# Optimization experiments

Measured on AMD Instinct MI355X. Metric: run time of the kernel, lower is better.

Reference implementation:

```python
import jax, jax.numpy as jnp
import numpy as np

EPS_BN = 1e-5


def _batchnorm(h, g, b):
    # training-mode BatchNorm1d over the flattened (B*N*k) axis
    mu = jnp.mean(h, axis=0)
    var = jnp.var(h, axis=0)
    return g * (h - mu) * jax.lax.rsqrt(var + EPS_BN) + b


def setup_inputs() -> dict:
    key = jax.random.key(0)
    ks = jax.random.split(key, 5)
    B, N = 4, 8192
    x = jax.random.normal(ks[0], (B, N, 3), dtype=jnp.float32)
    W1 = jax.random.normal(ks[1], (7, 10), dtype=jnp.float32) * (1.0 / np.sqrt(7.0))
    b1 = jax.random.normal(ks[2], (10,), dtype=jnp.float32) * 0.01
    W2 = jax.random.normal(ks[3], (10, 10), dtype=jnp.float32) * (1.0 / np.sqrt(10.0))
    b2 = jax.random.normal(ks[4], (10,), dtype=jnp.float32) * 0.01
    g1 = jnp.ones((10,), jnp.float32); be1 = jnp.zeros((10,), jnp.float32)
    g2 = jnp.ones((10,), jnp.float32); be2 = jnp.zeros((10,), jnp.float32)
    return {"x": x, "W1": W1, "b1": b1, "g1": g1, "be1": be1,
            "W2": W2, "b2": b2, "g2": g2, "be2": be2, "k": 9}


def reference(x, W1, b1, g1, be1, W2, b2, g2, be2, k):
    B, N, C = x.shape
    # --- kNN graph (brute force, self included as nearest) ---
    sq = jnp.sum(x * x, axis=-1)                                    # (B,N)
    d2 = sq[:, :, None] + sq[:, None, :] - 2.0 * jnp.einsum('bnc,bmc->bnm', x, x)
    _, idx = jax.lax.top_k(-d2, k + 1)                              # (B,N,k+1)
    nbrs = x[jnp.arange(B)[:, None, None], idx]                     # (B,N,k+1,3)
    rel = (nbrs - x[:, :, None, :])[:, :, 1:, :]                    # drop self -> (B,N,k,3)
    # --- sort neighbors by azimuth phi = atan2(y, x) ---
    phi = jnp.arctan2(rel[..., 1], rel[..., 0])                     # (B,N,k)
    order = jnp.argsort(phi, axis=-1)
    v1 = jnp.take_along_axis(rel, order[..., None], axis=2)         # (B,N,k,3)
    v2 = jnp.roll(v1, -1, axis=2)                                   # next neighbor (cyclic)
    # --- umbrella-style surface features ---
    centroids = 0.5 * (v1 + v2)
    normals = jnp.cross(v1, v2)
    normals = normals / (jnp.linalg.norm(normals, axis=-1, keepdims=True) + 1e-6)
    sign = jnp.where(normals[..., 0:1, 0] > 0, 1.0, -1.0)[..., None]  # (B,N,1,1)
    normals = normals * sign
    position = jnp.sum(normals * centroids, axis=-1, keepdims=True) / jnp.sqrt(jnp.asarray(3.0, x.dtype))
    feat = jnp.concatenate([centroids, normals, position], axis=-1)   # (B,N,k,7)
    feat = feat.reshape(B * N * k, 7)
    # --- tiny MLP + max-pool over k ---
    h = jax.nn.relu(_batchnorm(feat @ W1 + b1, g1, be1))
    h = jax.nn.relu(_batchnorm(h @ W2 + b2, g2, be2))
    return jnp.max(h.reshape(B, N, k, 10), axis=2)                  # (B,N,10)
```

## Files before the change

### kernel.cpp

```cpp
#include <hip/hip_runtime.h>
#include <math.h>
#include <float.h>
#include <stdint.h>

#define B_ 4
#define N_ 8192
#define K_ 9
#define NPTS (B_ * N_)
#define NROWS (NPTS * K_)
#define SPLIT 8
#define CHUNK (N_ / SPLIT)
#define NGROUP 32
#define GSIZE (CHUNK / NGROUP)
#define GSTRIDE 33
#define NCOPY 16

typedef float f4 __attribute__((ext_vector_type(4)));
typedef float f32x2 __attribute__((ext_vector_type(2)));

__device__ __forceinline__ f32x2 dist2_pk(f32x2 xx, f32x2 yy, f32x2 zz, f32x2 ww,
                                          f32x2 qx, f32x2 qy, f32x2 qz, f32x2 qw) {
  f32x2 t0 = qx * xx;
  f32x2 t1 = __builtin_elementwise_fma(qy, yy, t0);
  f32x2 t2 = __builtin_elementwise_fma(qz, zz, t1);
  f32x2 s  = qw + ww;
  f32x2 m2 = {-2.0f, -2.0f};
  return __builtin_elementwise_fma(t2, m2, s);
}

#define GDECL(G) float gd##G; int gi##G;
#define TOURN8()                                                           \
  float e01d, e23d, e45d, e67d, f03d, f47d, md;                            \
  int   e01i, e23i, e45i, e67i, f03i, f47i, mi;                            \
  { bool t;                                                                \
    t = d1 < d0; e01d = t ? d1 : d0; e01i = t ? (j + 1) : (j + 0);         \
    t = d3 < d2; e23d = t ? d3 : d2; e23i = t ? (j + 3) : (j + 2);         \
    t = d5 < d4; e45d = t ? d5 : d4; e45i = t ? (j + 5) : (j + 4);         \
    t = d7 < d6; e67d = t ? d7 : d6; e67i = t ? (j + 7) : (j + 6);         \
    t = e23d < e01d; f03d = t ? e23d : e01d; f03i = t ? e23i : e01i;       \
    t = e67d < e45d; f47d = t ? e67d : e45d; f47i = t ? e67i : e45i;       \
    t = f47d < f03d; md = t ? f47d : f03d; mi = t ? f47i : f03i; }
#define SCANG(G)                                                           \
  { float bgd = FLT_MAX; int bgi = 0;                                      \
    _Pragma("clang loop unroll(disable)")                                  \
    for (int pr = 0; pr < 16; pr += 4) {                                   \
      const f4* cp = CH + (G * GSTRIDE + 2 * pr);                          \
      f4 A0 = cp[0], B0 = cp[1], A1 = cp[2], B1 = cp[3];                   \
      f4 A2 = cp[4], B2 = cp[5], A3 = cp[6], B3 = cp[7];                   \
      int j = G * GSIZE + 2 * pr;                                          \
      f32x2 dA = dist2_pk(__builtin_shufflevector(A0, A0, 0, 1),           \
                          __builtin_shufflevector(A0, A0, 2, 3),           \
                          __builtin_shufflevector(B0, B0, 0, 1),           \
                          __builtin_shufflevector(B0, B0, 2, 3),           \
                          qx2, qy2, qz2, qw2);                             \
      f32x2 dB = dist2_pk(__builtin_shufflevector(A1, A1, 0, 1),           \
                          __builtin_shufflevector(A1, A1, 2, 3),           \
                          __builtin_shufflevector(B1, B1, 0, 1),           \
                          __builtin_shufflevector(B1, B1, 2, 3),           \
                          qx2, qy2, qz2, qw2);                             \
      f32x2 dC = dist2_pk(__builtin_shufflevector(A2, A2, 0, 1),           \
                          __builtin_shufflevector(A2, A2, 2, 3),           \
                          __builtin_shufflevector(B2, B2, 0, 1),           \
                          __builtin_shufflevector(B2, B2, 2, 3),           \
                          qx2, qy2, qz2, qw2);                             \
      f32x2 dD = dist2_pk(__builtin_shufflevector(A3, A3, 0, 1),           \
                          __builtin_shufflevector(A3, A3, 2, 3),           \
                          __builtin_shufflevector(B3, B3, 0, 1),           \
                          __builtin_shufflevector(B3, B3, 2, 3),           \
                          qx2, qy2, qz2, qw2);                             \
      float d0 = dA.x, d1 = dA.y, d2 = dB.x, d3 = dB.y;                    \
      float d4 = dC.x, d5 = dC.y, d6 = dD.x, d7 = dD.y;                    \
      if (HS) {                                                            \
        d0 = (j + 0 == nl) ? FLT_MAX : d0;                                 \
        d1 = (j + 1 == nl) ? FLT_MAX : d1;                                 \
        d2 = (j + 2 == nl) ? FLT_MAX : d2;                                 \
        d3 = (j + 3 == nl) ? FLT_MAX : d3;                                 \
        d4 = (j + 4 == nl) ? FLT_MAX : d4;                                 \
        d5 = (j + 5 == nl) ? FLT_MAX : d5;                                 \
        d6 = (j + 6 == nl) ? FLT_MAX : d6;                                 \
        d7 = (j + 7 == nl) ? FLT_MAX : d7;                                 \
      }                                                                    \
      TOURN8();                                                            \
      bool lt = md < bgd; bgd = lt ? md : bgd; bgi = lt ? mi : bgi;        \
    }                                                                      \
    gd##G = bgd; gi##G = bgi; }
#define LMC(G, S)                                                          \
  { bool lt = gd##G < wd##S;                                               \
    wd##S = lt ? gd##G : wd##S; wi##S = lt ? gi##G : wi##S;                \
    wg##S = lt ? G : wg##S; }
#define CMB(S)                                                             \
  { bool lt = wd##S < wda;                                                 \
    wda = lt ? wd##S : wda; wia = lt ? wi##S : wia; wga = lt ? wg##S : wga; }
#define WBK(G)                                                             \
  { bool m = (wg == G); gd##G = m ? nd : gd##G; gi##G = m ? ni : gi##G; }

template <bool HS>
__device__ __forceinline__ void knn_chunk(const f4* CH, f32x2 qx2, f32x2 qy2,
                                          f32x2 qz2, f32x2 qw2,
                                          int nl, int j0, int s, int p,
                                          uint2* __restrict__ PBDI) {
  GDECL(0) GDECL(1) GDECL(2) GDECL(3) GDECL(4) GDECL(5) GDECL(6) GDECL(7)
  GDECL(8) GDECL(9) GDECL(10) GDECL(11) GDECL(12) GDECL(13) GDECL(14) GDECL(15)
  GDECL(16) GDECL(17) GDECL(18) GDECL(19) GDECL(20) GDECL(21) GDECL(22) GDECL(23)
  GDECL(24) GDECL(25) GDECL(26) GDECL(27) GDECL(28) GDECL(29) GDECL(30) GDECL(31)

  SCANG(0) SCANG(1) SCANG(2) SCANG(3) SCANG(4) SCANG(5) SCANG(6) SCANG(7)
  SCANG(8) SCANG(9) SCANG(10) SCANG(11) SCANG(12) SCANG(13) SCANG(14) SCANG(15)
  SCANG(16) SCANG(17) SCANG(18) SCANG(19) SCANG(20) SCANG(21) SCANG(22) SCANG(23)
  SCANG(24) SCANG(25) SCANG(26) SCANG(27) SCANG(28) SCANG(29) SCANG(30) SCANG(31)

#pragma clang loop unroll(disable)
  for (int r = 0; r < K_; ++r) {
    float wda = gd0; int wia = gi0; int wga = 0;
    LMC(1,a) LMC(2,a) LMC(3,a) LMC(4,a) LMC(5,a) LMC(6,a) LMC(7,a)
    float wdb = gd8; int wib = gi8; int wgb = 8;
    LMC(9,b) LMC(10,b) LMC(11,b) LMC(12,b) LMC(13,b) LMC(14,b) LMC(15,b)
    float wdc = gd16; int wic = gi16; int wgc = 16;
    LMC(17,c) LMC(18,c) LMC(19,c) LMC(20,c) LMC(21,c) LMC(22,c) LMC(23,c)
    float wdd = gd24; int wid = gi24; int wgd = 24;
    LMC(25,d) LMC(26,d) LMC(27,d) LMC(28,d) LMC(29,d) LMC(30,d) LMC(31,d)
    CMB(b) CMB(c) CMB(d)
    float wd = wda; int wi = wia; int wg = wga;

    uint2 o; o.x = __float_as_uint(wd); o.y = (unsigned)(j0 + wi);
    PBDI[(size_t)(s * K_ + r) * NPTS + p] = o;

    int ab = wg * GSTRIDE;
    int jb = wg * GSIZE;
    float nd = FLT_MAX; int ni = 0;
#pragma clang loop unroll(disable)
    for (int pr = 0; pr < 16; pr += 4) {
      const f4* cp = CH + (ab + 2 * pr);
      f4 A0 = cp[0], B0 = cp[1], A1 = cp[2], B1 = cp[3];
      f4 A2 = cp[4], B2 = cp[5], A3 = cp[6], B3 = cp[7];
      int j = jb + 2 * pr;
      f32x2 dA = dist2_pk(__builtin_shufflevector(A0, A0, 0, 1),
                          __builtin_shufflevector(A0, A0, 2, 3),
                          __builtin_shufflevector(B0, B0, 0, 1),
                          __builtin_shufflevector(B0, B0, 2, 3),
                          qx2, qy2, qz2, qw2);
      f32x2 dB = dist2_pk(__builtin_shufflevector(A1, A1, 0, 1),
                          __builtin_shufflevector(A1, A1, 2, 3),
                          __builtin_shufflevector(B1, B1, 0, 1),
                          __builtin_shufflevector(B1, B1, 2, 3),
                          qx2, qy2, qz2, qw2);
      f32x2 dC = dist2_pk(__builtin_shufflevector(A2, A2, 0, 1),
                          __builtin_shufflevector(A2, A2, 2, 3),
                          __builtin_shufflevector(B2, B2, 0, 1),
                          __builtin_shufflevector(B2, B2, 2, 3),
                          qx2, qy2, qz2, qw2);
      f32x2 dD = dist2_pk(__builtin_shufflevector(A3, A3, 0, 1),
                          __builtin_shufflevector(A3, A3, 2, 3),
                          __builtin_shufflevector(B3, B3, 0, 1),
                          __builtin_shufflevector(B3, B3, 2, 3),
                          qx2, qy2, qz2, qw2);
      float d0 = dA.x, d1 = dA.y, d2 = dB.x, d3 = dB.y;
      float d4 = dC.x, d5 = dC.y, d6 = dD.x, d7 = dD.y;
      if (HS) {
        d0 = (j + 0 == nl) ? FLT_MAX : d0;
        d1 = (j + 1 == nl) ? FLT_MAX : d1;
        d2 = (j + 2 == nl) ? FLT_MAX : d2;
        d3 = (j + 3 == nl) ? FLT_MAX : d3;
        d4 = (j + 4 == nl) ? FLT_MAX : d4;
        d5 = (j + 5 == nl) ? FLT_MAX : d5;
        d6 = (j + 6 == nl) ? FLT_MAX : d6;
        d7 = (j + 7 == nl) ? FLT_MAX : d7;
      }
      bool k0 = (d0 > wd) | ((d0 == wd) & ((j + 0) > wi));
      bool k1 = (d1 > wd) | ((d1 == wd) & ((j + 1) > wi));
      bool k2 = (d2 > wd) | ((d2 == wd) & ((j + 2) > wi));
      bool k3 = (d3 > wd) | ((d3 == wd) & ((j + 3) > wi));
      bool k4 = (d4 > wd) | ((d4 == wd) & ((j + 4) > wi));
      bool k5 = (d5 > wd) | ((d5 == wd) & ((j + 5) > wi));
      bool k6 = (d6 > wd) | ((d6 == wd) & ((j + 6) > wi));
      bool k7 = (d7 > wd) | ((d7 == wd) & ((j + 7) > wi));
      d0 = k0 ? d0 : FLT_MAX;
      d1 = k1 ? d1 : FLT_MAX;
      d2 = k2 ? d2 : FLT_MAX;
      d3 = k3 ? d3 : FLT_MAX;
      d4 = k4 ? d4 : FLT_MAX;
      d5 = k5 ? d5 : FLT_MAX;
      d6 = k6 ? d6 : FLT_MAX;
      d7 = k7 ? d7 : FLT_MAX;
      TOURN8();
      bool lt = md < nd; nd = lt ? md : nd; ni = lt ? mi : ni;
    }
    WBK(0) WBK(1) WBK(2) WBK(3) WBK(4) WBK(5) WBK(6) WBK(7)
    WBK(8) WBK(9) WBK(10) WBK(11) WBK(12) WBK(13) WBK(14) WBK(15)
    WBK(16) WBK(17) WBK(18) WBK(19) WBK(20) WBK(21) WBK(22) WBK(23)
    WBK(24) WBK(25) WBK(26) WBK(27) WBK(28) WBK(29) WBK(30) WBK(31)
  }
}

__launch_bounds__(128, 4)
__global__ void k_knn(const float* __restrict__ x, uint2* __restrict__ PBDI) {
  __shared__ f4 CH[NGROUP * GSTRIDE];
  int bid = blockIdx.x;
  int pg = bid >> 3;
  int s = bid & (SPLIT - 1);
  int p = pg * 128 + threadIdx.x;
  int b = p >> 13;
  int n = p & (N_ - 1);
  int bO = b * N_;
  int j0 = s * CHUNK;

  const float* xq = x + 3 * (size_t)p;
  float qa = xq[0], qb = xq[1], qc = xq[2];
  float qw = qa * qa + qb * qb + qc * qc;
  f32x2 qx2 = {qa, qa}, qy2 = {qb, qb}, qz2 = {qc, qc}, qw2 = {qw, qw};

  for (int u = threadIdx.x; u < CHUNK / 2; u += 128) {
    const float* xp = x + 3 * (size_t)(bO + j0 + 2 * u);
    float a0 = xp[0], b0 = xp[1], c0 = xp[2];
    float a1 = xp[3], b1 = xp[4], c1 = xp[5];
    int G = u >> 4, rr = u & 15;
    f4 lo = {a0, a1, b0, b1};
    f4 hi = {c0, c1, a0 * a0 + b0 * b0 + c0 * c0, a1 * a1 + b1 * b1 + c1 * c1};
    CH[G * GSTRIDE + 2 * rr] = lo;
    CH[G * GSTRIDE + 2 * rr + 1] = hi;
  }
  __syncthreads();

  int n0 = (pg * 128) & (N_ - 1);
  int nl = n - j0;
  if (s == (n0 >> 10)) knn_chunk<true >(CH, qx2, qy2, qz2, qw2, nl, j0, s, p, PBDI);
  else                 knn_chunk<false>(CH, qx2, qy2, qz2, qw2, nl, j0, s, p, PBDI);
}

#define LVL(bdv, biv)                                                     \
  { bool lt = cd < (bdv); float td = (bdv); int ti = (biv);               \
    (bdv) = lt ? cd : (bdv); (biv) = lt ? ci : (biv);                     \
    cd = lt ? td : cd; ci = lt ? ti : ci; }
#define INS9ALL()                                                         \
  LVL(b0d, b0i) LVL(b1d, b1i) LVL(b2d, b2i) LVL(b3d, b3i) LVL(b4d, b4i)  \
  LVL(b5d, b5i) LVL(b6d, b6i) LVL(b7d, b7i) LVL(b8d, b8i)
#define TOP9_DECL()                                                       \
  float b0d = FLT_MAX, b1d = FLT_MAX, b2d = FLT_MAX, b3d = FLT_MAX,       \
        b4d = FLT_MAX, b5d = FLT_MAX, b6d = FLT_MAX, b7d = FLT_MAX,       \
        b8d = FLT_MAX;                                                    \
  int b0i = 0, b1i = 0, b2i = 0, b3i = 0, b4i = 0, b5i = 0, b6i = 0,      \
      b7i = 0, b8i = 0;

#define MKREL(T)                                                          \
  float rx##T, ry##T, rz##T, ph##T;                                       \
  { const float* mp = x + 3 * (size_t)(bO + b##T##i);                     \
    rx##T = mp[0] - qa; ry##T = mp[1] - qb; rz##T = mp[2] - qc;           \
    ph##T = atan2f(ry##T, rx##T); }

#define CE(A, Bv)                                                         \
  { bool lt = ph##Bv < ph##A; float t0;                                   \
    t0 = ph##A; ph##A = lt ? ph##Bv : t0; ph##Bv = lt ? t0 : ph##Bv;      \
    t0 = rx##A; rx##A = lt ? rx##Bv : t0; rx##Bv = lt ? t0 : rx##Bv;      \
    t0 = ry##A; ry##A = lt ? ry##Bv : t0; ry##Bv = lt ? t0 : ry##Bv;      \
    t0 = rz##A; rz##A = lt ? rz##Bv : t0; rz##Bv = lt ? t0 : rz##Bv; }

#define ST9(arr, v0, v1, v2, v3, v4, v5, v6, v7, v8)                      \
  arr[0 * 64 + pl] = v0; arr[1 * 64 + pl] = v1; arr[2 * 64 + pl] = v2;    \
  arr[3 * 64 + pl] = v3; arr[4 * 64 + pl] = v4; arr[5 * 64 + pl] = v5;    \
  arr[6 * 64 + pl] = v6; arr[7 * 64 + pl] = v7; arr[8 * 64 + pl] = v8;

__launch_bounds__(256, 4)
__global__ void k_tail1(const float* __restrict__ x, const uint2* __restrict__ PBDI,
                        const float* __restrict__ W1, const float* __restrict__ b1,
                        float* __restrict__ H1, double* __restrict__ ACC) {
  __shared__ float  LMD[64 * 37];
  __shared__ int    LMI[64 * 37];
  __shared__ float  LREL[3][9 * 64];
  __shared__ float  LSGN[64];
  __shared__ double sred[4][20];

  int q = threadIdx.x >> 6;
  int pl = threadIdx.x & 63;
  int pbase = blockIdx.x * 64;
  int p = pbase + pl;

  {
    TOP9_DECL();
#pragma clang loop unroll_count(2)
    for (int e = 0; e < 2 * K_; ++e) {
      uint2 v = PBDI[(size_t)(q * 2 * K_ + e) * NPTS + p];
      float cd = __uint_as_float(v.x);
      int ci = (int)v.y;
      INS9ALL();
    }
    int base = pl * 37 + q * 9;
    LMD[base + 0] = b0d; LMD[base + 1] = b1d; LMD[base + 2] = b2d;
    LMD[base + 3] = b3d; LMD[base + 4] = b4d; LMD[base + 5] = b5d;
    LMD[base + 6] = b6d; LMD[base + 7] = b7d; LMD[base + 8] = b8d;
    LMI[base + 0] = b0i; LMI[base + 1] = b1i; LMI[base + 2] = b2i;
    LMI[base + 3] = b3i; LMI[base + 4] = b4i; LMI[base + 5] = b5i;
    LMI[base + 6] = b6i; LMI[base + 7] = b7i; LMI[base + 8] = b8i;
  }
  __syncthreads();

  if (q == 0) {
    int b = p >> 13;
    int bO = b * N_;
    const float* xq = x + 3 * (size_t)p;
    float qa = xq[0], qb = xq[1], qc = xq[2];

    TOP9_DECL();
#pragma clang loop unroll_count(3)
    for (int e = 0; e < 4 * K_; ++e) {
      float cd = LMD[pl * 37 + e];
      int ci = LMI[pl * 37 + e];
      INS9ALL();
    }

    MKREL(0) MKREL(1) MKREL(2) MKREL(3) MKREL(4)
    MKREL(5) MKREL(6) MKREL(7) MKREL(8)

    CE(0,1)
    CE(1,2) CE(0,1)
    CE(2,3) CE(1,2) CE(0,1)
    CE(3,4) CE(2,3) CE(1,2) CE(0,1)
    CE(4,5) CE(3,4) CE(2,3) CE(1,2) CE(0,1)
    CE(5,6) CE(4,5) CE(3,4) CE(2,3) CE(1,2) CE(0,1)
    CE(6,7) CE(5,6) CE(4,5) CE(3,4) CE(2,3) CE(1,2) CE(0,1)
    CE(7,8) CE(6,7) CE(5,6) CE(4,5) CE(3,4) CE(2,3) CE(1,2) CE(0,1)

    float nx0 = ry0 * rz1 - rz0 * ry1;
    float ny0 = rz0 * rx1 - rx0 * rz1;
    float nz0 = rx0 * ry1 - ry0 * rx1;
    float nrm0 = sqrtf(nx0 * nx0 + ny0 * ny0 + nz0 * nz0) + 1e-6f;
    LSGN[pl] = ((nx0 / nrm0) > 0.0f) ? 1.0f : -1.0f;

    ST9(LREL[0], rx0, rx1, rx2, rx3, rx4, rx5, rx6, rx7, rx8)
    ST9(LREL[1], ry0, ry1, ry2, ry3, ry4, ry5, ry6, ry7, ry8)
    ST9(LREL[2], rz0, rz1, rz2, rz3, rz4, rz5, rz6, rz7, rz8)
  }
  __syncthreads();

  double sum[10], ss[10];
#pragma unroll
  for (int c = 0; c < 10; ++c) { sum[c] = 0.0; ss[c] = 0.0; }

#pragma clang loop unroll(disable)
  for (int rl = threadIdx.x; rl < 9 * 64; rl += 256) {
    int t = rl >> 6;
    int pp = rl & 63;
    int t2 = (t + 1 == K_) ? 0 : t + 1;
    float v1x = LREL[0][t * 64 + pp];
    float v1y = LREL[1][t * 64 + pp];
    float v1z = LREL[2][t * 64 + pp];
    float v2x = LREL[0][t2 * 64 + pp];
    float v2y = LREL[1][t2 * 64 + pp];
    float v2z = LREL[2][t2 * 64 + pp];
    float sgn = LSGN[pp];

    float cx = 0.5f * (v1x + v2x);
    float cy = 0.5f * (v1y + v2y);
    float cz = 0.5f * (v1z + v2z);
    float nx = v1y * v2z - v1z * v2y;
    float ny = v1z * v2x - v1x * v2z;
    float nz = v1x * v2y - v1y * v2x;
    float nrm = sqrtf(nx * nx + ny * ny + nz * nz) + 1e-6f;
    nx /= nrm; ny /= nrm; nz /= nrm;
    nx *= sgn; ny *= sgn; nz *= sgn;
    float pos = (nx * cx + ny * cy + nz * cz) / 1.7320508075688772f;

    float fv[7] = {cx, cy, cz, nx, ny, nz, pos};
#pragma unroll
    for (int c = 0; c < 10; ++c) {
      float h = b1[c];
#pragma unroll
      for (int rr = 0; rr < 7; ++rr) h = fmaf(fv[rr], W1[rr * 10 + c], h);
      H1[(size_t)c * NROWS + (size_t)t * NPTS + pbase + pp] = h;
      double hd = (double)h;
      sum[c] += hd; ss[c] += hd * hd;
    }
  }

  int lane = threadIdx.x & 63, wv = threadIdx.x >> 6;
#pragma unroll
  for (int c = 0; c < 10; ++c) {
    double a = sum[c];
#pragma unroll
    for (int off = 32; off > 0; off >>= 1) a += __shfl_down(a, off);
    if (lane == 0) sred[wv][c] = a;
    double qq = ss[c];
#pragma unroll
    for (int off = 32; off > 0; off >>= 1) qq += __shfl_down(qq, off);
    if (lane == 0) sred[wv][10 + c] = qq;
  }
  __syncthreads();
  if (threadIdx.x < 20) {
    atomicAdd(&ACC[(blockIdx.x & (NCOPY - 1)) * 40 + threadIdx.x],
              sred[0][threadIdx.x] + sred[1][threadIdx.x] +
              sred[2][threadIdx.x] + sred[3][threadIdx.x]);
  }
}

__launch_bounds__(64)
__global__ void k_mlp2(const float* __restrict__ H1, double* __restrict__ ACC,
                       const float* __restrict__ g1, const float* __restrict__ be1,
                       const float* __restrict__ W2, const float* __restrict__ b2,
                       const float* __restrict__ g2, float* __restrict__ EXT) {
  __shared__ float MR[20];
  __shared__ double sred[20];
  if (threadIdx.x < 20) {
    int c = threadIdx.x % 10;
    int half = threadIdx.x / 10;
    double s0 = 0.0, s1 = 0.0;
#pragma unroll
    for (int cc = 0; cc < NCOPY; ++cc) {
      s0 += ACC[cc * 40 + c];
      s1 += ACC[cc * 40 + 10 + c];
    }
    double mu = s0 / (double)NROWS;
    double var = s1 / (double)NROWS - mu * mu;
    MR[threadIdx.x] = half ? (float)(1.0 / sqrt(var + 1e-5)) : (float)mu;
  }
  __syncthreads();

  int p = blockIdx.x * 64 + threadIdx.x;
  double sum[10], ss[10];
  float ext[10], sg[10];
#pragma unroll
  for (int c = 0; c < 10; ++c) {
    sum[c] = 0.0; ss[c] = 0.0;
    sg[c] = g2[c];
    ext[c] = (sg[c] >= 0.0f) ? -FLT_MAX : FLT_MAX;
  }

#pragma clang loop unroll(disable)
  for (int t = 0; t < K_; ++t) {
    float v[10];
#pragma unroll
    for (int c = 0; c < 10; ++c) {
      float h = H1[(size_t)c * NROWS + (size_t)t * NPTS + p];
      float z = g1[c] * (h - MR[c]) * MR[10 + c] + be1[c];
      v[c] = z > 0.0f ? z : 0.0f;
    }
#pragma unroll
    for (int c = 0; c < 10; ++c) {
      float h = b2[c];
#pragma unroll
      for (int u = 0; u < 10; ++u) h = fmaf(v[u], W2[u * 10 + c], h);
      sum[c] += (double)h;
      ss[c] += (double)h * (double)h;
      ext[c] = (sg[c] >= 0.0f) ? fmaxf(ext[c], h) : fminf(ext[c], h);
    }
  }

#pragma unroll
  for (int c = 0; c < 10; ++c)
    EXT[(size_t)c * NPTS + p] = ext[c];

#pragma unroll
  for (int c = 0; c < 10; ++c) {
    double a = sum[c];
#pragma unroll
    for (int off = 32; off > 0; off >>= 1) a += __shfl_down(a, off);
    if (threadIdx.x == 0) sred[c] = a;
    double qq = ss[c];
#pragma unroll
    for (int off = 32; off > 0; off >>= 1) qq += __shfl_down(qq, off);
    if (threadIdx.x == 0) sred[10 + c] = qq;
  }
  __syncthreads();
  if (threadIdx.x < 20) {
    atomicAdd(&ACC[(blockIdx.x & (NCOPY - 1)) * 40 + 20 + threadIdx.x],
              sred[threadIdx.x]);
  }
}

__launch_bounds__(64)
__global__ void k_out(const float* __restrict__ EXT, const double* __restrict__ ACC,
                      const float* __restrict__ g2, const float* __restrict__ be2,
                      float* __restrict__ out) {
  __shared__ float MR[20];
  if (threadIdx.x < 20) {
    int c = threadIdx.x % 10;
    int half = threadIdx.x / 10;
    double s0 = 0.0, s1 = 0.0;
#pragma unroll
    for (int cc = 0; cc < NCOPY; ++cc) {
      s0 += ACC[cc * 40 + 20 + c];
      s1 += ACC[cc * 40 + 30 + c];
    }
    double mu = s0 / (double)NROWS;
    double var = s1 / (double)NROWS - mu * mu;
    MR[threadIdx.x] = half ? (float)(1.0 / sqrt(var + 1e-5)) : (float)mu;
  }
  __syncthreads();

  int p = blockIdx.x * 64 + threadIdx.x;
#pragma unroll
  for (int c = 0; c < 10; ++c) {
    float h = EXT[(size_t)c * NPTS + p];
    float z = g2[c] * (h - MR[c]) * MR[10 + c] + be2[c];
    z = z > 0.0f ? z : 0.0f;
    out[(size_t)p * 10 + c] = z;
  }
}

extern "C" void kernel_launch(void* const* d_in, const int* in_sizes, int n_in,
                              void* d_out, int out_size, void* d_ws, size_t ws_size,
                              hipStream_t stream) {
  (void)in_sizes; (void)n_in; (void)out_size; (void)ws_size;
  const float* x  = (const float*)d_in[0];
  const float* W1 = (const float*)d_in[1];
  const float* b1 = (const float*)d_in[2];
  const float* g1 = (const float*)d_in[3];
  const float* be1= (const float*)d_in[4];
  const float* W2 = (const float*)d_in[5];
  const float* b2 = (const float*)d_in[6];
  const float* g2 = (const float*)d_in[7];
  const float* be2= (const float*)d_in[8];
  float* out = (float*)d_out;

  char* base = (char*)d_ws;
  uint2*  PBDI = (uint2*)base;
  float*  H1 = (float*)(base + (size_t)SPLIT * K_ * NPTS * 8);
  double* ACC = (double*)(H1 + (size_t)10 * NROWS);
  float*  EXT = (float*)PBDI;

  hipMemsetAsync(ACC, 0, NCOPY * 40 * sizeof(double), stream);
  k_knn<<<(NPTS / 128) * SPLIT, 128, 0, stream>>>(x, PBDI);
  k_tail1<<<NPTS / 64, 256, 0, stream>>>(x, PBDI, W1, b1, H1, ACC);
  k_mlp2<<<NPTS / 64, 64, 0, stream>>>(H1, ACC, g1, be1, W2, b2, g2, EXT);
  k_out<<<NPTS / 64, 64, 0, stream>>>(EXT, ACC, g2, be2, out);
}
```

Baseline: 231.6 us.

## Defer kNN index tracking to winner recompute, fold ACC memset into kernel, unroll loops

The brute-force kNN scan now keeps only the min distance per 8-candidate batch with fminf, plus the batch position, and no longer carries indices through a tournament. Each time a group wins a selection round, its winning batch is recomputed to find the exact index, taking the lowest index on ties. This is meant to cut ALU and register work in the hot distance-scan loop, at the cost of a small extra recompute per selected neighbour. Separately, the ACC zeroing moves from a hipMemsetAsync into block 0 of k_knn to save a launch, and two tail loops are fully unrolled.

```diff
diff --git a/kernel.cpp b/kernel.cpp
--- a/kernel.cpp
+++ b/kernel.cpp
@@ -29,25 +29,13 @@
 }
 
 #define GDECL(G) float gd##G; int gi##G;
-#define TOURN8()                                                           \
-  float e01d, e23d, e45d, e67d, f03d, f47d, md;                            \
-  int   e01i, e23i, e45i, e67i, f03i, f47i, mi;                            \
-  { bool t;                                                                \
-    t = d1 < d0; e01d = t ? d1 : d0; e01i = t ? (j + 1) : (j + 0);         \
-    t = d3 < d2; e23d = t ? d3 : d2; e23i = t ? (j + 3) : (j + 2);         \
-    t = d5 < d4; e45d = t ? d5 : d4; e45i = t ? (j + 5) : (j + 4);         \
-    t = d7 < d6; e67d = t ? d7 : d6; e67i = t ? (j + 7) : (j + 6);         \
-    t = e23d < e01d; f03d = t ? e23d : e01d; f03i = t ? e23i : e01i;       \
-    t = e67d < e45d; f47d = t ? e67d : e45d; f47i = t ? e67i : e45i;       \
-    t = f47d < f03d; md = t ? f47d : f03d; mi = t ? f47i : f03i; }
 #define SCANG(G)                                                           \
-  { float bgd = FLT_MAX; int bgi = 0;                                      \
+  { float bgd = FLT_MAX; int bq = 0;                                       \
     _Pragma("clang loop unroll(disable)")                                  \
     for (int pr = 0; pr < 16; pr += 4) {                                   \
       const f4* cp = CH + (G * GSTRIDE + 2 * pr);                          \
       f4 A0 = cp[0], B0 = cp[1], A1 = cp[2], B1 = cp[3];                   \
       f4 A2 = cp[4], B2 = cp[5], A3 = cp[6], B3 = cp[7];                   \
-      int j = G * GSIZE + 2 * pr;                                          \
       f32x2 dA = dist2_pk(__builtin_shufflevector(A0, A0, 0, 1),           \
                           __builtin_shufflevector(A0, A0, 2, 3),           \
                           __builtin_shufflevector(B0, B0, 0, 1),           \
@@ -71,6 +59,7 @@
       float d0 = dA.x, d1 = dA.y, d2 = dB.x, d3 = dB.y;                    \
       float d4 = dC.x, d5 = dC.y, d6 = dD.x, d7 = dD.y;                    \
       if (HS) {                                                            \
+        int j = G * GSIZE + 2 * pr;                                        \
         d0 = (j + 0 == nl) ? FLT_MAX : d0;                                 \
         d1 = (j + 1 == nl) ? FLT_MAX : d1;                                 \
         d2 = (j + 2 == nl) ? FLT_MAX : d2;                                 \
@@ -80,10 +69,11 @@
         d6 = (j + 6 == nl) ? FLT_MAX : d6;                                 \
         d7 = (j + 7 == nl) ? FLT_MAX : d7;                                 \
       }                                                                    \
-      TOURN8();                                                            \
-      bool lt = md < bgd; bgd = lt ? md : bgd; bgi = lt ? mi : bgi;        \
+      float m = fminf(fminf(fminf(d0, d1), fminf(d2, d3)),                 \
+                      fminf(fminf(d4, d5), fminf(d6, d7)));                \
+      bool lt = m < bgd; bgd = lt ? m : bgd; bq = lt ? pr : bq;            \
     }                                                                      \
-    gd##G = bgd; gi##G = bgi; }
+    gd##G = bgd; gi##G = -1 - bq; }
 #define LMC(G, S)                                                          \
   { bool lt = gd##G < wd##S;                                               \
     wd##S = lt ? gd##G : wd##S; wi##S = lt ? gi##G : wi##S;                \
@@ -93,6 +83,18 @@
     wda = lt ? wd##S : wda; wia = lt ? wi##S : wia; wga = lt ? wg##S : wga; }
 #define WBK(G)                                                             \
   { bool m = (wg == G); gd##G = m ? nd : gd##G; gi##G = m ? ni : gi##G; }
+
+#define TOURN8()                                                           \
+  float e01d, e23d, e45d, e67d, f03d, f47d, md;                            \
+  int   e01i, e23i, e45i, e67i, f03i, f47i, mi;                            \
+  { bool t;                                                                \
+    t = d1 < d0; e01d = t ? d1 : d0; e01i = t ? (j + 1) : (j + 0);         \
+    t = d3 < d2; e23d = t ? d3 : d2; e23i = t ? (j + 3) : (j + 2);         \
+    t = d5 < d4; e45d = t ? d5 : d4; e45i = t ? (j + 5) : (j + 4);         \
+    t = d7 < d6; e67d = t ? d7 : d6; e67i = t ? (j + 7) : (j + 6);         \
+    t = e23d < e01d; f03d = t ? e23d : e01d; f03i = t ? e23i : e01i;       \
+    t = e67d < e45d; f47d = t ? e67d : e45d; f47i = t ? e67i : e45i;       \
+    t = f47d < f03d; md = t ? f47d : f03d; mi = t ? f47i : f03i; }
 
 template <bool HS>
 __device__ __forceinline__ void knn_chunk(const f4* CH, f32x2 qx2, f32x2 qy2,
@@ -120,13 +122,72 @@
     float wdd = gd24; int wid = gi24; int wgd = 24;
     LMC(25,d) LMC(26,d) LMC(27,d) LMC(28,d) LMC(29,d) LMC(30,d) LMC(31,d)
     CMB(b) CMB(c) CMB(d)
-    float wd = wda; int wi = wia; int wg = wga;
+    float wd = wda; int wist = wia; int wg = wga;
+
+    int ab = wg * GSTRIDE;
+    int jb = wg * GSIZE;
+
+    int wi;
+    {
+      int bq = (wist >= 0) ? 0 : (-1 - wist);
+      const f4* cp = CH + (ab + 2 * bq);
+      f4 A0 = cp[0], B0 = cp[1], A1 = cp[2], B1 = cp[3];
+      f4 A2 = cp[4], B2 = cp[5], A3 = cp[6], B3 = cp[7];
+      int j = jb + 2 * bq;
+      f32x2 dA = dist2_pk(__builtin_shufflevector(A0, A0, 0, 1),
+                          __builtin_shufflevector(A0, A0, 2, 3),
+                          __builtin_shufflevector(B0, B0, 0, 1),
+                          __builtin_shufflevector(B0, B0, 2, 3),
+                          qx2, qy2, qz2, qw2);
+      f32x2 dB = dist2_pk(__builtin_shufflevector(A1, A1, 0, 1),
+                          __builtin_shufflevector(A1, A1, 2, 3),
+                          __builtin_shufflevector(B1, B1, 0, 1),
+                          __builtin_shufflevector(B1, B1, 2, 3),
+                          qx2, qy2, qz2, qw2);
+      f32x2 dC = dist2_pk(__builtin_shufflevector(A2, A2, 0, 1),
+                          __builtin_shufflevector(A2, A2, 2, 3),
+                          __builtin_shufflevector(B2, B2, 0, 1),
+                          __builtin_shufflevector(B2, B2, 2, 3),
+                          qx2, qy2, qz2, qw2);
+      f32x2 dD = dist2_pk(__builtin_shufflevector(A3, A3, 0, 1),
+                          __builtin_shufflevector(A3, A3, 2, 3),
+                          __builtin_shufflevector(B3, B3, 0, 1),
+                          __builtin_shufflevector(B3, B3, 2, 3),
+                          qx2, qy2, qz2, qw2);
+      float d0 = dA.x, d1 = dA.y, d2 = dB.x, d3 = dB.y;
+      float d4 = dC.x, d5 = dC.y, d6 = dD.x, d7 = dD.y;
+      if (HS) {
+        d0 = (j + 0 == nl) ? FLT_MAX : d0;
+        d1 = (j + 1 == nl) ? FLT_MAX : d1;
+        d2 = (j + 2 == nl) ? FLT_MAX : d2;
+        d3 = (j + 3 == nl) ? FLT_MAX : d3;
+        d4 = (j + 4 == nl) ? FLT_MAX : d4;
+        d5 = (j + 5 == nl) ? FLT_MAX : d5;
+        d6 = (j + 6 == nl) ? FLT_MAX : d6;
+        d7 = (j + 7 == nl) ? FLT_MAX : d7;
+      }
+      const int IMX = 0x7fffffff;
+      int a0 = (d0 == wd) ? (j + 0) : IMX;
+      int a1 = (d1 == wd) ? (j + 1) : IMX;
+      int a2 = (d2 == wd) ? (j + 2) : IMX;
+      int a3 = (d3 == wd) ? (j + 3) : IMX;
+      int a4 = (d4 == wd) ? (j + 4) : IMX;
+      int a5 = (d5 == wd) ? (j + 5) : IMX;
+      int a6 = (d6 == wd) ? (j + 6) : IMX;
+      int a7 = (d7 == wd) ? (j + 7) : IMX;
+      int m01 = a0 < a1 ? a0 : a1;
+      int m23 = a2 < a3 ? a2 : a3;
+      int m45 = a4 < a5 ? a4 : a5;
+      int m67 = a6 < a7 ? a6 : a7;
+      int mA = m01 < m23 ? m01 : m23;
+      int mB = m45 < m67 ? m45 : m67;
+      int jm = mA < mB ? mA : mB;
+      wi = (wist >= 0) ? wist : jm;
+    }
 
     uint2 o; o.x = __float_as_uint(wd); o.y = (unsigned)(j0 + wi);
     PBDI[(size_t)(s * K_ + r) * NPTS + p] = o;
 
-    int ab = wg * GSTRIDE;
-    int jb = wg * GSIZE;
     float nd = FLT_MAX; int ni = 0;
 #pragma clang loop unroll(disable)
     for (int pr = 0; pr < 16; pr += 4) {
@@ -193,9 +254,13 @@
 }
 
 __launch_bounds__(128, 4)
-__global__ void k_knn(const float* __restrict__ x, uint2* __restrict__ PBDI) {
+__global__ void k_knn(const float* __restrict__ x, uint2* __restrict__ PBDI,
+                      double* __restrict__ ACC) {
   __shared__ f4 CH[NGROUP * GSTRIDE];
   int bid = blockIdx.x;
+  if (bid == 0) {
+    for (int t = threadIdx.x; t < NCOPY * 40; t += 128) ACC[t] = 0.0;
+  }
   int pg = bid >> 3;
   int s = bid & (SPLIT - 1);
   int p = pg * 128 + threadIdx.x;
@@ -276,7 +341,7 @@
 
   {
     TOP9_DECL();
-#pragma clang loop unroll_count(2)
+#pragma unroll
     for (int e = 0; e < 2 * K_; ++e) {
       uint2 v = PBDI[(size_t)(q * 2 * K_ + e) * NPTS + p];
       float cd = __uint_as_float(v.x);
@@ -423,7 +488,7 @@
     ext[c] = (sg[c] >= 0.0f) ? -FLT_MAX : FLT_MAX;
   }
 
-#pragma clang loop unroll(disable)
+#pragma unroll
   for (int t = 0; t < K_; ++t) {
     float v[10];
 #pragma unroll
@@ -516,8 +581,7 @@
   double* ACC = (double*)(H1 + (size_t)10 * NROWS);
   float*  EXT = (float*)PBDI;
 
-  hipMemsetAsync(ACC, 0, NCOPY * 40 * sizeof(double), stream);
-  k_knn<<<(NPTS / 128) * SPLIT, 128, 0, stream>>>(x, PBDI);
+  k_knn<<<(NPTS / 128) * SPLIT, 128, 0, stream>>>(x, PBDI, ACC);
   k_tail1<<<NPTS / 64, 256, 0, stream>>>(x, PBDI, W1, b1, H1, ACC);
   k_mlp2<<<NPTS / 64, 64, 0, stream>>>(H1, ACC, g1, be1, W2, b2, g2, EXT);
   k_out<<<NPTS / 64, 64, 0, stream>>>(EXT, ACC, g2, be2, out);
```

After: 259.1 us. 1.12x slower.
